# Performance work log

Measured on AMD Instinct MI355X. Metric: run time of the kernel, lower is better.

## Reference

```python
import jax, jax.numpy as jnp
import numpy as np

NX, NY = 384, 384
H = 1e-4
DT = 5e-9
NT = 192
STRIDE = 4
RHO = 1610.0
F0 = 2.0e6
T0 = 4e-7
AMP = 1e10
GAUSS_A = 5e6

C11_INIT, C22_INIT, C12_INIT = 1.3074e11, 1.15e10, 1.049e10
C16_INIT, C26_INIT, C66_INIT = 3.067e10, 3.75e9, 1.477e10
B11 = (5e10, 2.5e11); B22 = (5e9, 5e10); B12 = (5e9, 5e10)
B16 = (0.0, 6e10); B26 = (0.0, 2e10); B66 = (5e9, 3e10)


def setup_inputs() -> dict:
    # log-parameter fields, constant-initialized as in the module __init__
    full = lambda v: jnp.full((1, NX, NY), np.log(v), dtype=jnp.float32)
    log_C11 = full(C11_INIT)
    log_C22 = full(C22_INIT)
    log_C12 = full(C12_INIT)
    log_C16 = full(abs(C16_INIT) + 1e6)
    log_C26 = full(abs(C26_INIT) + 1e6)
    log_C66 = full(C66_INIT)
    # Gaussian point-load distribution centered at domain center
    Lx, Ly = H * (NX - 1), H * (NY - 1)
    x = np.linspace(-Lx / 2, Lx / 2, NX)
    y = np.linspace(-Ly / 2, Ly / 2, NY)
    X, Y = np.meshgrid(x, y, indexing='ij')
    gauss = (GAUSS_A / np.pi) * np.exp(-GAUSS_A * (X ** 2 + Y ** 2))
    # Ricker wavelet source signal over nt steps
    t = np.arange(NT) * DT
    tau = t - T0
    pft2 = (np.pi * F0 * tau) ** 2
    sig = AMP * (1.0 - 2.0 * pft2) * np.exp(-pft2)
    return {
        'log_C11': log_C11, 'log_C12': log_C12, 'log_C16': log_C16,
        'log_C22': log_C22, 'log_C26': log_C26, 'log_C66': log_C66,
        'gaussian_dist': jnp.asarray(gauss, dtype=jnp.float32),
        'source_signal': jnp.asarray(sig, dtype=jnp.float32),
    }


def _stencils(u, hinv2):
    # u: (B, nx, ny). Zero padding == fixed (u=0) boundary, matching conv2d_fixed.
    up = jnp.pad(u, ((0, 0), (1, 1), (1, 1)))
    d2x = (up[:, :-2, 1:-1] - 2.0 * u + up[:, 2:, 1:-1]) * hinv2
    d2y = (up[:, 1:-1, :-2] - 2.0 * u + up[:, 1:-1, 2:]) * hinv2
    dxy = 0.25 * (up[:, :-2, :-2] - up[:, :-2, 2:] - up[:, 2:, :-2] + up[:, 2:, 2:]) * hinv2
    return d2x, d2y, dxy


def _simulate(log_C11, log_C12, log_C16, log_C22, log_C26, log_C66,
              gaussian_dist, source_signal):
    clip = lambda lc, b: jnp.clip(jnp.exp(lc), b[0], b[1])
    C11 = clip(log_C11, B11); C22 = clip(log_C22, B22); C12 = clip(log_C12, B12)
    C16 = clip(log_C16, B16); C26 = clip(log_C26, B26); C66 = clip(log_C66, B66)
    hinv2 = jnp.float32(1.0 / (H * H))
    dt2 = jnp.float32(DT * DT)
    g = gaussian_dist[None]  # (1, nx, ny)
    C12p66 = C12 + C66

    def step(carry, sig_t):
        ux1, uy1, ux2, uy2 = carry
        dxx_x, dyy_x, dxy_x = _stencils(ux1, hinv2)
        dxx_y, dyy_y, dxy_y = _stencils(uy1, hinv2)
        Lux = (C11 * dxx_x + C66 * dyy_x + C12p66 * dxy_y
               + 2.0 * C16 * dxy_x + C16 * dxx_y + C26 * dyy_y)
        Luy = (C66 * dxx_y + C22 * dyy_y + C12p66 * dxy_x
               + C16 * dxx_x + C26 * dyy_x + 2.0 * C26 * dxy_y)
        # Ricker point source on the y-component (source_component='y')
        ax = Lux / RHO
        ay = (Luy + sig_t * g) / RHO
        ux_new = 2.0 * ux1 - ux2 + dt2 * ax
        uy_new = 2.0 * uy1 - uy2 + dt2 * ay
        return (ux_new, uy_new, ux1, uy1), (ux_new, uy_new)

    z = jnp.zeros((1, NX, NY), dtype=jnp.float32)
    _, (ux_all, uy_all) = jax.lax.scan(step, (z, z, z, z), source_signal)
    # subsample by primary_time_stride -> (1, nt//stride, nx, ny)
    ux_f = jnp.transpose(ux_all[STRIDE - 1::STRIDE], (1, 0, 2, 3))
    uy_f = jnp.transpose(uy_all[STRIDE - 1::STRIDE], (1, 0, 2, 3))
    return jnp.stack([ux_f, uy_f])  # (2, 1, nt_out, nx, ny)


def reference(log_C11, log_C12, log_C16, log_C22, log_C26, log_C66,
              gaussian_dist, source_signal):
    return _simulate(log_C11, log_C12, log_C16, log_C22, log_C26, log_C66,
                     gaussian_dist, source_signal)
```

## Files before the change

### kernel.cpp

```cpp
#include <hip/hip_runtime.h>


typedef float v2f __attribute__((ext_vector_type(2)));

#define NXg 384
#define NYg 384
#define NPT (NXg * NYg)
#define NFRAMES 48

#define OWN 24
#define HALO 12
#define TS 48
#define KSTEPS 12
#define NLAUNCH 16

#define H_   1e-4
#define DT_  5e-9
#define RHO_ 1610.0

#define B11_LO 5e10f
#define B11_HI 2.5e11f
#define B22_LO 5e9f
#define B22_HI 5e10f
#define B12_LO 5e9f
#define B12_HI 5e10f
#define B16_LO 0.0f
#define B16_HI 6e10f
#define B26_LO 0.0f
#define B26_HI 2e10f
#define B66_LO 5e9f
#define B66_HI 3e10f

static __device__ __constant__ float kScale  = (float)(DT_ * DT_ / (H_ * H_) / RHO_);
static __device__ __constant__ float kSrcScl = (float)(DT_ * DT_ / RHO_);

__device__ __forceinline__ float clipf(float v, float lo, float hi) {
    return fminf(fmaxf(v, lo), hi);
}
__device__ __forceinline__ v2f vfma(v2f a, v2f b, v2f c) {
    return __builtin_elementwise_fma(a, b, c);
}
__device__ __forceinline__ v2f vbc(float s) { v2f r; r[0] = s; r[1] = s; return r; }
__device__ __forceinline__ v2f vswap(v2f a) { return __builtin_shufflevector(a, a, 1, 0); }

#define LDS_BARRIER() asm volatile("s_waitcnt lgkmcnt(0)\n\ts_barrier" ::: "memory")


__global__ __launch_bounds__(256)
void setup_kernel(const float* __restrict__ lc11, const float* __restrict__ lc12,
                  const float* __restrict__ lc16, const float* __restrict__ lc22,
                  const float* __restrict__ lc26, const float* __restrict__ lc66,
                  const float* __restrict__ gauss, float* __restrict__ ws) {
    int i = blockIdx.x * blockDim.x + threadIdx.x;
    if (i >= NPT) return;
    float C11 = clipf(expf(lc11[i]), B11_LO, B11_HI);
    float C12 = clipf(expf(lc12[i]), B12_LO, B12_HI);
    float C16 = clipf(expf(lc16[i]), B16_LO, B16_HI);
    float C22 = clipf(expf(lc22[i]), B22_LO, B22_HI);
    float C26 = clipf(expf(lc26[i]), B26_LO, B26_HI);
    float C66 = clipf(expf(lc66[i]), B66_LO, B66_HI);
    float s = kScale;
    float4* C0 = (float4*)ws;
    float4* C1 = (float4*)(ws + 4 * (size_t)NPT);
    C0[i] = make_float4(C11 * s, C22 * s, (C12 + C66) * s, C16 * s);
    C1[i] = make_float4(C26 * s, C66 * s, gauss[i] * kSrcScl, 0.0f);
    float4* s0 = (float4*)(ws + 8 * (size_t)NPT);
    s0[i] = make_float4(0.0f, 0.0f, 0.0f, 0.0f);
}

__global__ __launch_bounds__(256, 1)
void fused_kernel(const float* __restrict__ ws, const float* __restrict__ sig,
                  const float4* __restrict__ inS, float4* __restrict__ outS,
                  float* __restrict__ out, int L) {
    __shared__ v2f sb[2][TS][TS + 1];

    const int tid = threadIdx.x;
    const int tx = tid >> 4;
    const int ty = tid & 15;
    const int r0 = 3 * tx;
    const int c0 = 3 * ty;
    const int gx0 = blockIdx.y * OWN - HALO;
    const int gy0 = blockIdx.x * OWN - HALO;

    const float4* __restrict__ C0 = (const float4*)ws;
    const float4* __restrict__ C1 = (const float4*)(ws + 4 * (size_t)NPT);

    v2f cur[9], old_[9];
    v2f ca[9], cb[9];
    float a12p66[9], a16[9], a26[9], gs[9];
    int gidx[9];

#pragma unroll
    for (int i = 0; i < 3; ++i) {
#pragma unroll
        for (int j = 0; j < 3; ++j) {
            int p = i * 3 + j;
            int gx = gx0 + r0 + i;
            int gy = gy0 + c0 + j;
            bool d = (unsigned)gx < (unsigned)NXg && (unsigned)gy < (unsigned)NYg;
            int g = d ? gx * NYg + gy : 0;
            gidx[p] = g;
            float4 st = d ? inS[g] : make_float4(0, 0, 0, 0);
            v2f c; c[0] = st.x; c[1] = st.y;
            v2f o; o[0] = st.z; o[1] = st.w;
            cur[p] = c; old_[p] = o;
            float4 k0 = d ? C0[g] : make_float4(0, 0, 0, 0);
            float4 k1 = d ? C1[g] : make_float4(0, 0, 0, 0);
            v2f t; t[0] = k0.x; t[1] = k1.y; ca[p] = t;
            v2f u; u[0] = k1.y; u[1] = k0.y; cb[p] = u;
            a12p66[p] = k0.z; a16[p] = k0.w; a26[p] = k1.x; gs[p] = k1.z;
        }
    }

    const int t0 = L * KSTEPS;
    float sigv[KSTEPS];
#pragma unroll
    for (int k = 0; k < KSTEPS; ++k) sigv[k] = sig[t0 + k];

    const int rm = (r0 > 0) ? r0 - 1 : 0;
    const int rp = (r0 + 3 < TS) ? r0 + 3 : TS - 1;
    const int cm = (c0 > 0) ? c0 - 1 : 0;
    const int cp = (c0 + 3 < TS) ? c0 + 3 : TS - 1;

    const bool owned = (tx >= 4) && (tx < 12) && (ty >= 4) && (ty < 12);

#pragma unroll
    for (int i = 0; i < 3; ++i)
#pragma unroll
        for (int j = 0; j < 3; ++j)
            sb[0][r0 + i][c0 + j] = cur[i * 3 + j];
    LDS_BARRIER();

    v2f c20; c20[0] = 2.0f; c20[1] = 0.0f;
    v2f c02; c02[0] = 0.0f; c02[1] = 2.0f;
    const v2f m2 = vbc(-2.0f);
    const v2f qt = vbc(0.25f);
    const v2f two = vbc(2.0f);

#pragma unroll 1
    for (int s = 1; s <= KSTEPS; ++s) {
        const v2f (*rb)[TS + 1] = sb[(s - 1) & 1];
        v2f (*wb)[TS + 1] = sb[s & 1];
        v2f vsig; vsig[0] = 0.0f; vsig[1] = sigv[s - 1];

        v2f v[5][5];
#pragma unroll
        for (int i = 0; i < 3; ++i)
#pragma unroll
            for (int j = 0; j < 3; ++j)
                v[i + 1][j + 1] = cur[i * 3 + j];
        v[0][0] = rb[rm][cm];  v[0][4] = rb[rm][cp];
        v[4][0] = rb[rp][cm];  v[4][4] = rb[rp][cp];
#pragma unroll
        for (int j = 0; j < 3; ++j) {
            v[0][j + 1] = rb[rm][c0 + j];
            v[4][j + 1] = rb[rp][c0 + j];
            v[j + 1][0] = rb[r0 + j][cm];
            v[j + 1][4] = rb[r0 + j][cp];
        }

        v2f dh[5][3];
#pragma unroll
        for (int i = 0; i < 5; ++i)
#pragma unroll
            for (int j = 0; j < 3; ++j)
                dh[i][j] = v[i][j + 2] - v[i][j];

#pragma unroll
        for (int i = 0; i < 3; ++i)
#pragma unroll
            for (int j = 0; j < 3; ++j) {
                int p = i * 3 + j;
                v2f c = v[i + 1][j + 1];
                v2f sxx = vfma(m2, c, v[i][j + 1] + v[i + 2][j + 1]);
                v2f syy = vfma(m2, c, v[i + 1][j] + v[i + 1][j + 2]);
                v2f sxy = qt * (dh[i + 2][j] - dh[i][j]);

                v2f t4 = vfma(c20, vbc(sxy[0]), vswap(sxx));
                v2f t5 = vfma(c02, vbc(sxy[1]), vswap(syy));
                v2f Lv = ca[p] * sxx;
                Lv = vfma(cb[p], syy, Lv);
                Lv = vfma(vbc(a12p66[p]), vswap(sxy), Lv);
                Lv = vfma(vbc(a16[p]), t4, Lv);
                Lv = vfma(vbc(a26[p]), t5, Lv);
                Lv = vfma(vsig, vbc(gs[p]), Lv);
                v2f n = vfma(two, c, Lv) - old_[p];
                old_[p] = c;
                cur[p] = n;
            }

        if ((s & 3) == 0 && owned) {
            int f = 3 * L + (s >> 2) - 1;
            float* oux = out + (size_t)f * NPT;
            float* ouy = out + (size_t)(NFRAMES + f) * NPT;
#pragma unroll
            for (int p = 0; p < 9; ++p) {
                oux[gidx[p]] = cur[p][0];
                ouy[gidx[p]] = cur[p][1];
            }
        }

#pragma unroll
        for (int i = 0; i < 3; ++i)
#pragma unroll
            for (int j = 0; j < 3; ++j)
                wb[r0 + i][c0 + j] = cur[i * 3 + j];
        LDS_BARRIER();
    }

    if (owned) {
#pragma unroll
        for (int p = 0; p < 9; ++p) {
            float4 st = make_float4(cur[p][0], cur[p][1], old_[p][0], old_[p][1]);
            outS[gidx[p]] = st;
        }
    }
}

extern "C" void kernel_launch(void* const* d_in, const int* in_sizes, int n_in,
                              void* d_out, int out_size, void* d_ws, size_t ws_size,
                              hipStream_t stream) {
    const float* lc11  = (const float*)d_in[0];
    const float* lc12  = (const float*)d_in[1];
    const float* lc16  = (const float*)d_in[2];
    const float* lc22  = (const float*)d_in[3];
    const float* lc26  = (const float*)d_in[4];
    const float* lc66  = (const float*)d_in[5];
    const float* gauss = (const float*)d_in[6];
    const float* sig   = (const float*)d_in[7];

    float* ws  = (float*)d_ws;
    float* out = (float*)d_out;

    setup_kernel<<<(NPT + 255) / 256, 256, 0, stream>>>(lc11, lc12, lc16, lc22,
                                                        lc26, lc66, gauss, ws);

    float4* set0 = (float4*)(ws + 8 * (size_t)NPT);
    float4* set1 = (float4*)(ws + 12 * (size_t)NPT);

    dim3 grid(NXg / OWN, NYg / OWN);
    for (int L = 0; L < NLAUNCH; ++L) {
        float4* iS = (L & 1) ? set1 : set0;
        float4* oS = (L & 1) ? set0 : set1;
        fused_kernel<<<grid, 256, 0, stream>>>(ws, sig, iS, oS, out, L);
    }
}
```

Before: 353.7 us.

## Replace per-epoch kernel launches with a persistent cooperative kernel using grid sync

The 16 separate launches of the temporally blocked stencil kernel become one cooperative persistent kernel that loops over epochs and uses grid.sync() between them. Owned cells keep their state in registers across epochs, and only halo cells reload from the global ping-pong state buffers. This targets launch overhead and the reload of coefficients and interior state on every launch. In exchange it depends on all 256 blocks being co-resident and adds grid-wide barrier latency.

After: 817.2 us. 131% more time.

```diff
diff --git a/kernel.cpp b/kernel.cpp
--- a/kernel.cpp
+++ b/kernel.cpp
@@ -1,4 +1,7 @@
 #include <hip/hip_runtime.h>
+#include <hip/hip_cooperative_groups.h>
+
+namespace cg = cooperative_groups;
 
 
 typedef float v2f __attribute__((ext_vector_type(2)));
@@ -12,7 +15,7 @@
 #define HALO 12
 #define TS 48
 #define KSTEPS 12
-#define NLAUNCH 16
+#define NEPOCH 16
 
 #define H_   1e-4
 #define DT_  5e-9
@@ -65,13 +68,16 @@
     C0[i] = make_float4(C11 * s, C22 * s, (C12 + C66) * s, C16 * s);
     C1[i] = make_float4(C26 * s, C66 * s, gauss[i] * kSrcScl, 0.0f);
     float4* s0 = (float4*)(ws + 8 * (size_t)NPT);
+    float4* s1 = (float4*)(ws + 12 * (size_t)NPT);
     s0[i] = make_float4(0.0f, 0.0f, 0.0f, 0.0f);
+    s1[i] = make_float4(0.0f, 0.0f, 0.0f, 0.0f);
 }
 
 __global__ __launch_bounds__(256, 1)
-void fused_kernel(const float* __restrict__ ws, const float* __restrict__ sig,
-                  const float4* __restrict__ inS, float4* __restrict__ outS,
-                  float* __restrict__ out, int L) {
+void persist_kernel(float* __restrict__ ws, const float* __restrict__ sig,
+                    float* __restrict__ out) {
+    cg::grid_group grid = cg::this_grid();
+
     __shared__ v2f sb[2][TS][TS + 1];
 
     const int tid = threadIdx.x;
@@ -84,11 +90,15 @@
 
     const float4* __restrict__ C0 = (const float4*)ws;
     const float4* __restrict__ C1 = (const float4*)(ws + 4 * (size_t)NPT);
+    float4* __restrict__ st[2];
+    st[0] = (float4*)(ws + 8 * (size_t)NPT);
+    st[1] = (float4*)(ws + 12 * (size_t)NPT);
 
     v2f cur[9], old_[9];
     v2f ca[9], cb[9];
     float a12p66[9], a16[9], a26[9], gs[9];
     int gidx[9];
+    bool dom[9];
 
 #pragma unroll
     for (int i = 0; i < 3; ++i) {
@@ -99,23 +109,16 @@
             int gy = gy0 + c0 + j;
             bool d = (unsigned)gx < (unsigned)NXg && (unsigned)gy < (unsigned)NYg;
             int g = d ? gx * NYg + gy : 0;
-            gidx[p] = g;
-            float4 st = d ? inS[g] : make_float4(0, 0, 0, 0);
-            v2f c; c[0] = st.x; c[1] = st.y;
-            v2f o; o[0] = st.z; o[1] = st.w;
-            cur[p] = c; old_[p] = o;
+            gidx[p] = g; dom[p] = d;
             float4 k0 = d ? C0[g] : make_float4(0, 0, 0, 0);
             float4 k1 = d ? C1[g] : make_float4(0, 0, 0, 0);
             v2f t; t[0] = k0.x; t[1] = k1.y; ca[p] = t;
             v2f u; u[0] = k1.y; u[1] = k0.y; cb[p] = u;
             a12p66[p] = k0.z; a16[p] = k0.w; a26[p] = k1.x; gs[p] = k1.z;
+            cur[p] = vbc(0.0f);
+            old_[p] = vbc(0.0f);
         }
     }
-
-    const int t0 = L * KSTEPS;
-    float sigv[KSTEPS];
-#pragma unroll
-    for (int k = 0; k < KSTEPS; ++k) sigv[k] = sig[t0 + k];
 
     const int rm = (r0 > 0) ? r0 - 1 : 0;
     const int rp = (r0 + 3 < TS) ? r0 + 3 : TS - 1;
@@ -123,13 +126,6 @@
     const int cp = (c0 + 3 < TS) ? c0 + 3 : TS - 1;
 
     const bool owned = (tx >= 4) && (tx < 12) && (ty >= 4) && (ty < 12);
-
-#pragma unroll
-    for (int i = 0; i < 3; ++i)
-#pragma unroll
-        for (int j = 0; j < 3; ++j)
-            sb[0][r0 + i][c0 + j] = cur[i * 3 + j];
-    LDS_BARRIER();
 
     v2f c20; c20[0] = 2.0f; c20[1] = 0.0f;
     v2f c02; c02[0] = 0.0f; c02[1] = 2.0f;
@@ -138,81 +134,111 @@
     const v2f two = vbc(2.0f);
 
 #pragma unroll 1
-    for (int s = 1; s <= KSTEPS; ++s) {
-        const v2f (*rb)[TS + 1] = sb[(s - 1) & 1];
-        v2f (*wb)[TS + 1] = sb[s & 1];
-        v2f vsig; vsig[0] = 0.0f; vsig[1] = sigv[s - 1];
-
-        v2f v[5][5];
+    for (int e = 0; e < NEPOCH; ++e) {
+        if (!owned) {
+            const float4* __restrict__ rs = st[(e + 1) & 1];
+#pragma unroll
+            for (int p = 0; p < 9; ++p) {
+                float4 s4 = dom[p] ? rs[gidx[p]] : make_float4(0, 0, 0, 0);
+                v2f c; c[0] = s4.x; c[1] = s4.y;
+                v2f o; o[0] = s4.z; o[1] = s4.w;
+                cur[p] = c; old_[p] = o;
+            }
+        }
+        const int t0 = e * KSTEPS;
+        float sigv[KSTEPS];
+#pragma unroll
+        for (int k = 0; k < KSTEPS; ++k) sigv[k] = sig[t0 + k];
+
 #pragma unroll
         for (int i = 0; i < 3; ++i)
 #pragma unroll
             for (int j = 0; j < 3; ++j)
-                v[i + 1][j + 1] = cur[i * 3 + j];
-        v[0][0] = rb[rm][cm];  v[0][4] = rb[rm][cp];
-        v[4][0] = rb[rp][cm];  v[4][4] = rb[rp][cp];
-#pragma unroll
-        for (int j = 0; j < 3; ++j) {
-            v[0][j + 1] = rb[rm][c0 + j];
-            v[4][j + 1] = rb[rp][c0 + j];
-            v[j + 1][0] = rb[r0 + j][cm];
-            v[j + 1][4] = rb[r0 + j][cp];
-        }
-
-        v2f dh[5][3];
-#pragma unroll
-        for (int i = 0; i < 5; ++i)
-#pragma unroll
-            for (int j = 0; j < 3; ++j)
-                dh[i][j] = v[i][j + 2] - v[i][j];
-
-#pragma unroll
-        for (int i = 0; i < 3; ++i)
+                sb[0][r0 + i][c0 + j] = cur[i * 3 + j];
+        LDS_BARRIER();
+
+#pragma unroll 1
+        for (int s = 1; s <= KSTEPS; ++s) {
+            const v2f (*rb)[TS + 1] = sb[(s - 1) & 1];
+            v2f (*wb)[TS + 1] = sb[s & 1];
+            v2f vsig; vsig[0] = 0.0f; vsig[1] = sigv[s - 1];
+
+            v2f v[5][5];
+#pragma unroll
+            for (int i = 0; i < 3; ++i)
+#pragma unroll
+                for (int j = 0; j < 3; ++j)
+                    v[i + 1][j + 1] = cur[i * 3 + j];
+            v[0][0] = rb[rm][cm];  v[0][4] = rb[rm][cp];
+            v[4][0] = rb[rp][cm];  v[4][4] = rb[rp][cp];
 #pragma unroll
             for (int j = 0; j < 3; ++j) {
-                int p = i * 3 + j;
-                v2f c = v[i + 1][j + 1];
-                v2f sxx = vfma(m2, c, v[i][j + 1] + v[i + 2][j + 1]);
-                v2f syy = vfma(m2, c, v[i + 1][j] + v[i + 1][j + 2]);
-                v2f sxy = qt * (dh[i + 2][j] - dh[i][j]);
-
-                v2f t4 = vfma(c20, vbc(sxy[0]), vswap(sxx));
-                v2f t5 = vfma(c02, vbc(sxy[1]), vswap(syy));
-                v2f Lv = ca[p] * sxx;
-                Lv = vfma(cb[p], syy, Lv);
-                Lv = vfma(vbc(a12p66[p]), vswap(sxy), Lv);
-                Lv = vfma(vbc(a16[p]), t4, Lv);
-                Lv = vfma(vbc(a26[p]), t5, Lv);
-                Lv = vfma(vsig, vbc(gs[p]), Lv);
-                v2f n = vfma(two, c, Lv) - old_[p];
-                old_[p] = c;
-                cur[p] = n;
-            }
-
-        if ((s & 3) == 0 && owned) {
-            int f = 3 * L + (s >> 2) - 1;
-            float* oux = out + (size_t)f * NPT;
-            float* ouy = out + (size_t)(NFRAMES + f) * NPT;
-#pragma unroll
-            for (int p = 0; p < 9; ++p) {
-                oux[gidx[p]] = cur[p][0];
-                ouy[gidx[p]] = cur[p][1];
-            }
-        }
-
-#pragma unroll
-        for (int i = 0; i < 3; ++i)
-#pragma unroll
-            for (int j = 0; j < 3; ++j)
-                wb[r0 + i][c0 + j] = cur[i * 3 + j];
-        LDS_BARRIER();
-    }
-
-    if (owned) {
-#pragma unroll
-        for (int p = 0; p < 9; ++p) {
-            float4 st = make_float4(cur[p][0], cur[p][1], old_[p][0], old_[p][1]);
-            outS[gidx[p]] = st;
+                v[0][j + 1] = rb[rm][c0 + j];
+                v[4][j + 1] = rb[rp][c0 + j];
+                v[j + 1][0] = rb[r0 + j][cm];
+                v[j + 1][4] = rb[r0 + j][cp];
+            }
+
+            v2f dh[5][3];
+#pragma unroll
+            for (int i = 0; i < 5; ++i)
+#pragma unroll
+                for (int j = 0; j < 3; ++j)
+                    dh[i][j] = v[i][j + 2] - v[i][j];
+
+#pragma unroll
+            for (int i = 0; i < 3; ++i)
+#pragma unroll
+                for (int j = 0; j < 3; ++j) {
+                    int p = i * 3 + j;
+                    v2f c = v[i + 1][j + 1];
+                    v2f sxx = vfma(m2, c, v[i][j + 1] + v[i + 2][j + 1]);
+                    v2f syy = vfma(m2, c, v[i + 1][j] + v[i + 1][j + 2]);
+                    v2f sxy = qt * (dh[i + 2][j] - dh[i][j]);
+
+                    v2f t4 = vfma(c20, vbc(sxy[0]), vswap(sxx));
+                    v2f t5 = vfma(c02, vbc(sxy[1]), vswap(syy));
+                    v2f Lv = ca[p] * sxx;
+                    Lv = vfma(cb[p], syy, Lv);
+                    Lv = vfma(vbc(a12p66[p]), vswap(sxy), Lv);
+                    Lv = vfma(vbc(a16[p]), t4, Lv);
+                    Lv = vfma(vbc(a26[p]), t5, Lv);
+                    Lv = vfma(vsig, vbc(gs[p]), Lv);
+                    v2f n = vfma(two, c, Lv) - old_[p];
+                    old_[p] = c;
+                    cur[p] = n;
+                }
+
+            if ((s & 3) == 0 && owned) {
+                int f = 3 * e + (s >> 2) - 1;
+                float* oux = out + (size_t)f * NPT;
+                float* ouy = out + (size_t)(NFRAMES + f) * NPT;
+#pragma unroll
+                for (int p = 0; p < 9; ++p) {
+                    oux[gidx[p]] = cur[p][0];
+                    ouy[gidx[p]] = cur[p][1];
+                }
+            }
+
+#pragma unroll
+            for (int i = 0; i < 3; ++i)
+#pragma unroll
+                for (int j = 0; j < 3; ++j)
+                    wb[r0 + i][c0 + j] = cur[i * 3 + j];
+            LDS_BARRIER();
+        }
+
+        if (e + 1 < NEPOCH) {
+            if (owned) {
+                float4* __restrict__ wsbuf = st[e & 1];
+#pragma unroll
+                for (int p = 0; p < 9; ++p) {
+                    float4 s4 = make_float4(cur[p][0], cur[p][1],
+                                            old_[p][0], old_[p][1]);
+                    wsbuf[gidx[p]] = s4;
+                }
+            }
+            grid.sync();
         }
     }
 }
@@ -235,13 +261,8 @@
     setup_kernel<<<(NPT + 255) / 256, 256, 0, stream>>>(lc11, lc12, lc16, lc22,
                                                         lc26, lc66, gauss, ws);
 
-    float4* set0 = (float4*)(ws + 8 * (size_t)NPT);
-    float4* set1 = (float4*)(ws + 12 * (size_t)NPT);
-
+    void* args[] = {(void*)&ws, (void*)&sig, (void*)&out};
     dim3 grid(NXg / OWN, NYg / OWN);
-    for (int L = 0; L < NLAUNCH; ++L) {
-        float4* iS = (L & 1) ? set1 : set0;
-        float4* oS = (L & 1) ? set0 : set1;
-        fused_kernel<<<grid, 256, 0, stream>>>(ws, sig, iS, oS, out, L);
-    }
-}
+    hipLaunchCooperativeKernel((void*)persist_kernel, grid, dim3(256), args, 0,
+                               stream);
+}
```

## Replace LDS tile exchange with per-wave row strips and DPP lane shifts

Applied to the files above, without the earlier changes.

The thread mapping changes from 3x3 point blocks to one column per lane, with each wavefront owning a 12-row strip. Neighbours along y now come from DPP lane shifts, and only the strip's boundary rows go through a small LDS buffer, with one barrier per step. This removes most LDS traffic and the scattered halo reads of the old shared tile. In exchange, 16 of every 64 lanes sit idle, and the code depends on DPP wave-shift support on the target hardware.

Result: slower. 391.4 us (+10.7%).

```diff
diff --git a/kernel.cpp b/kernel.cpp
--- a/kernel.cpp
+++ b/kernel.cpp
@@ -13,6 +13,7 @@
 #define TS 48
 #define KSTEPS 12
 #define NLAUNCH 16
+#define ROWS 12
 
 #define H_   1e-4
 #define DT_  5e-9
@@ -42,6 +43,23 @@
 }
 __device__ __forceinline__ v2f vbc(float s) { v2f r; r[0] = s; r[1] = s; return r; }
 __device__ __forceinline__ v2f vswap(v2f a) { return __builtin_shufflevector(a, a, 1, 0); }
+
+__device__ __forceinline__ float dpp_from_lo(float x) {
+    int v = __builtin_amdgcn_update_dpp(0, __builtin_bit_cast(int, x),
+                                        0x138, 0xf, 0xf, true);
+    return __builtin_bit_cast(float, v);
+}
+__device__ __forceinline__ float dpp_from_hi(float x) {
+    int v = __builtin_amdgcn_update_dpp(0, __builtin_bit_cast(int, x),
+                                        0x130, 0xf, 0xf, true);
+    return __builtin_bit_cast(float, v);
+}
+__device__ __forceinline__ v2f shiftL(v2f a) {
+    v2f r; r[0] = dpp_from_lo(a[0]); r[1] = dpp_from_lo(a[1]); return r;
+}
+__device__ __forceinline__ v2f shiftR(v2f a) {
+    v2f r; r[0] = dpp_from_hi(a[0]); r[1] = dpp_from_hi(a[1]); return r;
+}
 
 #define LDS_BARRIER() asm volatile("s_waitcnt lgkmcnt(0)\n\ts_barrier" ::: "memory")
 
@@ -72,44 +90,38 @@
 void fused_kernel(const float* __restrict__ ws, const float* __restrict__ sig,
                   const float4* __restrict__ inS, float4* __restrict__ outS,
                   float* __restrict__ out, int L) {
-    __shared__ v2f sb[2][TS][TS + 1];
+    __shared__ v2f xch[2][4][2][64];
 
     const int tid = threadIdx.x;
-    const int tx = tid >> 4;
-    const int ty = tid & 15;
-    const int r0 = 3 * tx;
-    const int c0 = 3 * ty;
-    const int gx0 = blockIdx.y * OWN - HALO;
-    const int gy0 = blockIdx.x * OWN - HALO;
+    const int w = tid >> 6;
+    const int c = tid & 63;
+    const int gx0 = (int)blockIdx.y * OWN - HALO;
+    const int gy = (int)blockIdx.x * OWN - HALO + c;
 
     const float4* __restrict__ C0 = (const float4*)ws;
     const float4* __restrict__ C1 = (const float4*)(ws + 4 * (size_t)NPT);
 
-    v2f cur[9], old_[9];
-    v2f ca[9], cb[9];
-    float a12p66[9], a16[9], a26[9], gs[9];
-    int gidx[9];
-
-#pragma unroll
-    for (int i = 0; i < 3; ++i) {
-#pragma unroll
-        for (int j = 0; j < 3; ++j) {
-            int p = i * 3 + j;
-            int gx = gx0 + r0 + i;
-            int gy = gy0 + c0 + j;
-            bool d = (unsigned)gx < (unsigned)NXg && (unsigned)gy < (unsigned)NYg;
-            int g = d ? gx * NYg + gy : 0;
-            gidx[p] = g;
-            float4 st = d ? inS[g] : make_float4(0, 0, 0, 0);
-            v2f c; c[0] = st.x; c[1] = st.y;
-            v2f o; o[0] = st.z; o[1] = st.w;
-            cur[p] = c; old_[p] = o;
-            float4 k0 = d ? C0[g] : make_float4(0, 0, 0, 0);
-            float4 k1 = d ? C1[g] : make_float4(0, 0, 0, 0);
-            v2f t; t[0] = k0.x; t[1] = k1.y; ca[p] = t;
-            v2f u; u[0] = k1.y; u[1] = k0.y; cb[p] = u;
-            a12p66[p] = k0.z; a16[p] = k0.w; a26[p] = k1.x; gs[p] = k1.z;
-        }
+    v2f cur[ROWS], old_[ROWS];
+    v2f ca[ROWS], cb[ROWS];
+    float a12p66[ROWS], a16[ROWS], a26[ROWS], gs[ROWS];
+    int g[ROWS];
+
+    const bool colOk = (c < TS) && ((unsigned)gy < (unsigned)NYg);
+#pragma unroll
+    for (int r = 0; r < ROWS; ++r) {
+        int gx = gx0 + ROWS * w + r;
+        bool d = colOk && ((unsigned)gx < (unsigned)NXg);
+        int gg = d ? gx * NYg + gy : 0;
+        g[r] = gg;
+        float4 st = d ? inS[gg] : make_float4(0, 0, 0, 0);
+        v2f cc; cc[0] = st.x; cc[1] = st.y;
+        v2f oo; oo[0] = st.z; oo[1] = st.w;
+        cur[r] = cc; old_[r] = oo;
+        float4 k0 = d ? C0[gg] : make_float4(0, 0, 0, 0);
+        float4 k1 = d ? C1[gg] : make_float4(0, 0, 0, 0);
+        v2f t; t[0] = k0.x; t[1] = k1.y; ca[r] = t;
+        v2f u; u[0] = k1.y; u[1] = k0.y; cb[r] = u;
+        a12p66[r] = k0.z; a16[r] = k0.w; a26[r] = k1.x; gs[r] = k1.z;
     }
 
     const int t0 = L * KSTEPS;
@@ -117,19 +129,10 @@
 #pragma unroll
     for (int k = 0; k < KSTEPS; ++k) sigv[k] = sig[t0 + k];
 
-    const int rm = (r0 > 0) ? r0 - 1 : 0;
-    const int rp = (r0 + 3 < TS) ? r0 + 3 : TS - 1;
-    const int cm = (c0 > 0) ? c0 - 1 : 0;
-    const int cp = (c0 + 3 < TS) ? c0 + 3 : TS - 1;
-
-    const bool owned = (tx >= 4) && (tx < 12) && (ty >= 4) && (ty < 12);
-
-#pragma unroll
-    for (int i = 0; i < 3; ++i)
-#pragma unroll
-        for (int j = 0; j < 3; ++j)
-            sb[0][r0 + i][c0 + j] = cur[i * 3 + j];
-    LDS_BARRIER();
+    const bool ownW = (w == 1) || (w == 2);
+    const bool ownC = (c >= HALO) && (c < HALO + OWN);
+    const int wa = (w > 0) ? w - 1 : w;
+    const int wb = (w < 3) ? w + 1 : w;
 
     v2f c20; c20[0] = 2.0f; c20[1] = 0.0f;
     v2f c02; c02[0] = 0.0f; c02[1] = 2.0f;
@@ -139,81 +142,69 @@
 
 #pragma unroll 1
     for (int s = 1; s <= KSTEPS; ++s) {
-        const v2f (*rb)[TS + 1] = sb[(s - 1) & 1];
-        v2f (*wb)[TS + 1] = sb[s & 1];
+        v2f (*xb)[2][64] = xch[s & 1];
+        xb[w][0][c] = cur[0];
+        xb[w][1][c] = cur[ROWS - 1];
+        LDS_BARRIER();
+        v2f Ba = xb[wa][1][c];
+        v2f Bb = xb[wb][0][c];
+        if (w == 0) Ba = vbc(0.0f);
+        if (w == 3) Bb = vbc(0.0f);
+
         v2f vsig; vsig[0] = 0.0f; vsig[1] = sigv[s - 1];
 
-        v2f v[5][5];
-#pragma unroll
-        for (int i = 0; i < 3; ++i)
-#pragma unroll
-            for (int j = 0; j < 3; ++j)
-                v[i + 1][j + 1] = cur[i * 3 + j];
-        v[0][0] = rb[rm][cm];  v[0][4] = rb[rm][cp];
-        v[4][0] = rb[rp][cm];  v[4][4] = rb[rp][cp];
-#pragma unroll
-        for (int j = 0; j < 3; ++j) {
-            v[0][j + 1] = rb[rm][c0 + j];
-            v[4][j + 1] = rb[rp][c0 + j];
-            v[j + 1][0] = rb[r0 + j][cm];
-            v[j + 1][4] = rb[r0 + j][cp];
+        v2f slA = shiftL(Ba), srA = shiftR(Ba);
+        v2f Dprev = slA - srA;
+        v2f below_prev = Ba;
+        v2f sl0 = shiftL(cur[0]), sr0 = shiftR(cur[0]);
+        v2f Dcur = sl0 - sr0;
+        v2f Scur = sl0 + sr0;
+
+#pragma unroll
+        for (int r = 0; r < ROWS; ++r) {
+            v2f nxt = (r < ROWS - 1) ? cur[r + 1] : Bb;
+            v2f sln = shiftL(nxt), srn = shiftR(nxt);
+            v2f Dnext = sln - srn;
+            v2f Snext = sln + srn;
+
+            v2f cc = cur[r];
+            v2f sxx = vfma(m2, cc, below_prev + nxt);
+            v2f syy = vfma(m2, cc, Scur);
+            v2f sxy = qt * (Dprev - Dnext);
+
+            v2f t4 = vfma(c20, vbc(sxy[0]), vswap(sxx));
+            v2f t5 = vfma(c02, vbc(sxy[1]), vswap(syy));
+            v2f Lv = ca[r] * sxx;
+            Lv = vfma(cb[r], syy, Lv);
+            Lv = vfma(vbc(a12p66[r]), vswap(sxy), Lv);
+            Lv = vfma(vbc(a16[r]), t4, Lv);
+            Lv = vfma(vbc(a26[r]), t5, Lv);
+            Lv = vfma(vsig, vbc(gs[r]), Lv);
+            v2f n = vfma(two, cc, Lv) - old_[r];
+
+            old_[r] = cc;
+            cur[r] = n;
+            below_prev = cc;
+            Dprev = Dcur; Dcur = Dnext; Scur = Snext;
         }
 
-        v2f dh[5][3];
-#pragma unroll
-        for (int i = 0; i < 5; ++i)
-#pragma unroll
-            for (int j = 0; j < 3; ++j)
-                dh[i][j] = v[i][j + 2] - v[i][j];
-
-#pragma unroll
-        for (int i = 0; i < 3; ++i)
-#pragma unroll
-            for (int j = 0; j < 3; ++j) {
-                int p = i * 3 + j;
-                v2f c = v[i + 1][j + 1];
-                v2f sxx = vfma(m2, c, v[i][j + 1] + v[i + 2][j + 1]);
-                v2f syy = vfma(m2, c, v[i + 1][j] + v[i + 1][j + 2]);
-                v2f sxy = qt * (dh[i + 2][j] - dh[i][j]);
-
-                v2f t4 = vfma(c20, vbc(sxy[0]), vswap(sxx));
-                v2f t5 = vfma(c02, vbc(sxy[1]), vswap(syy));
-                v2f Lv = ca[p] * sxx;
-                Lv = vfma(cb[p], syy, Lv);
-                Lv = vfma(vbc(a12p66[p]), vswap(sxy), Lv);
-                Lv = vfma(vbc(a16[p]), t4, Lv);
-                Lv = vfma(vbc(a26[p]), t5, Lv);
-                Lv = vfma(vsig, vbc(gs[p]), Lv);
-                v2f n = vfma(two, c, Lv) - old_[p];
-                old_[p] = c;
-                cur[p] = n;
-            }
-
-        if ((s & 3) == 0 && owned) {
+        if ((s & 3) == 0 && ownW && ownC) {
             int f = 3 * L + (s >> 2) - 1;
             float* oux = out + (size_t)f * NPT;
             float* ouy = out + (size_t)(NFRAMES + f) * NPT;
 #pragma unroll
-            for (int p = 0; p < 9; ++p) {
-                oux[gidx[p]] = cur[p][0];
-                ouy[gidx[p]] = cur[p][1];
+            for (int r = 0; r < ROWS; ++r) {
+                oux[g[r]] = cur[r][0];
+                ouy[g[r]] = cur[r][1];
             }
         }
-
-#pragma unroll
-        for (int i = 0; i < 3; ++i)
-#pragma unroll
-            for (int j = 0; j < 3; ++j)
-                wb[r0 + i][c0 + j] = cur[i * 3 + j];
-        LDS_BARRIER();
-    }
-
-    if (owned) {
-#pragma unroll
-        for (int p = 0; p < 9; ++p) {
-            float4 st = make_float4(cur[p][0], cur[p][1], old_[p][0], old_[p][1]);
-            outS[gidx[p]] = st;
-        }
+    }
+
+    if (ownW && ownC) {
+#pragma unroll
+        for (int r = 0; r < ROWS; ++r)
+            outS[g[r]] = make_float4(cur[r][0], cur[r][1],
+                                     old_[r][0], old_[r][1]);
     }
 }
 
```

## Use 512-thread blocks with 2x3 points per thread and a taller halo tile

Applied to the files above, without the earlier changes.

Each block now runs 512 threads over a 64x48 LDS tile. Each thread owns 2x3 points instead of 3x3, and the row halo grows from 12 to 20 so the thread grid divides the tile evenly. The goal is twice the waves per CU and fewer registers per thread, to hide LDS and ALU latency in the time-stepping loop. The cost is about a third more redundant halo computation per block. The final step's LDS write and barrier are also skipped, since nothing reads them.

After: 373.2 us. 1.05x slower.

```diff
diff --git a/kernel.cpp b/kernel.cpp
--- a/kernel.cpp
+++ b/kernel.cpp
@@ -9,10 +9,13 @@
 #define NFRAMES 48
 
 #define OWN 24
-#define HALO 12
-#define TS 48
+#define HALOR 20
+#define HALOC 12
+#define TSR 64
+#define TSC 48
 #define KSTEPS 12
 #define NLAUNCH 16
+#define SCOL 49
 
 #define H_   1e-4
 #define DT_  5e-9
@@ -68,30 +71,30 @@
     s0[i] = make_float4(0.0f, 0.0f, 0.0f, 0.0f);
 }
 
-__global__ __launch_bounds__(256, 1)
+__global__ __launch_bounds__(512)
 void fused_kernel(const float* __restrict__ ws, const float* __restrict__ sig,
                   const float4* __restrict__ inS, float4* __restrict__ outS,
                   float* __restrict__ out, int L) {
-    __shared__ v2f sb[2][TS][TS + 1];
+    __shared__ v2f sb[2][TSR][SCOL];
 
     const int tid = threadIdx.x;
-    const int tx = tid >> 4;
-    const int ty = tid & 15;
-    const int r0 = 3 * tx;
-    const int c0 = 3 * ty;
-    const int gx0 = blockIdx.y * OWN - HALO;
-    const int gy0 = blockIdx.x * OWN - HALO;
+    const int rg = tid >> 4;
+    const int cg = tid & 15;
+    const int r0 = 2 * rg;
+    const int c0 = 3 * cg;
+    const int gx0 = (int)blockIdx.y * OWN - HALOR;
+    const int gy0 = (int)blockIdx.x * OWN - HALOC;
 
     const float4* __restrict__ C0 = (const float4*)ws;
     const float4* __restrict__ C1 = (const float4*)(ws + 4 * (size_t)NPT);
 
-    v2f cur[9], old_[9];
-    v2f ca[9], cb[9];
-    float a12p66[9], a16[9], a26[9], gs[9];
-    int gidx[9];
-
-#pragma unroll
-    for (int i = 0; i < 3; ++i) {
+    v2f cur[6], old_[6];
+    v2f ca[6], cb[6];
+    float a12p66[6], a16[6], a26[6], gs[6];
+    int gidx[6];
+
+#pragma unroll
+    for (int i = 0; i < 2; ++i) {
 #pragma unroll
         for (int j = 0; j < 3; ++j) {
             int p = i * 3 + j;
@@ -118,14 +121,14 @@
     for (int k = 0; k < KSTEPS; ++k) sigv[k] = sig[t0 + k];
 
     const int rm = (r0 > 0) ? r0 - 1 : 0;
-    const int rp = (r0 + 3 < TS) ? r0 + 3 : TS - 1;
+    const int rp = (r0 + 2 < TSR) ? r0 + 2 : TSR - 1;
     const int cm = (c0 > 0) ? c0 - 1 : 0;
-    const int cp = (c0 + 3 < TS) ? c0 + 3 : TS - 1;
-
-    const bool owned = (tx >= 4) && (tx < 12) && (ty >= 4) && (ty < 12);
-
-#pragma unroll
-    for (int i = 0; i < 3; ++i)
+    const int cp = (c0 + 3 < TSC) ? c0 + 3 : TSC - 1;
+
+    const bool owned = (rg >= 10) && (rg < 22) && (cg >= 4) && (cg < 12);
+
+#pragma unroll
+    for (int i = 0; i < 2; ++i)
 #pragma unroll
         for (int j = 0; j < 3; ++j)
             sb[0][r0 + i][c0 + j] = cur[i * 3 + j];
@@ -139,42 +142,43 @@
 
 #pragma unroll 1
     for (int s = 1; s <= KSTEPS; ++s) {
-        const v2f (*rb)[TS + 1] = sb[(s - 1) & 1];
-        v2f (*wb)[TS + 1] = sb[s & 1];
+        const v2f (*rb)[SCOL] = sb[(s - 1) & 1];
+        v2f (*wb)[SCOL] = sb[s & 1];
         v2f vsig; vsig[0] = 0.0f; vsig[1] = sigv[s - 1];
 
-        v2f v[5][5];
-#pragma unroll
-        for (int i = 0; i < 3; ++i)
+        v2f v[4][5];
+#pragma unroll
+        for (int i = 0; i < 2; ++i)
 #pragma unroll
             for (int j = 0; j < 3; ++j)
                 v[i + 1][j + 1] = cur[i * 3 + j];
         v[0][0] = rb[rm][cm];  v[0][4] = rb[rm][cp];
-        v[4][0] = rb[rp][cm];  v[4][4] = rb[rp][cp];
+        v[3][0] = rb[rp][cm];  v[3][4] = rb[rp][cp];
 #pragma unroll
         for (int j = 0; j < 3; ++j) {
             v[0][j + 1] = rb[rm][c0 + j];
-            v[4][j + 1] = rb[rp][c0 + j];
-            v[j + 1][0] = rb[r0 + j][cm];
-            v[j + 1][4] = rb[r0 + j][cp];
-        }
-
-        v2f dh[5][3];
-#pragma unroll
-        for (int i = 0; i < 5; ++i)
+            v[3][j + 1] = rb[rp][c0 + j];
+        }
+        v[1][0] = rb[r0][cm];      v[1][4] = rb[r0][cp];
+        v[2][0] = rb[r0 + 1][cm];  v[2][4] = rb[r0 + 1][cp];
+
+        v2f dh[4][3];
+#pragma unroll
+        for (int i = 0; i < 4; ++i)
 #pragma unroll
             for (int j = 0; j < 3; ++j)
                 dh[i][j] = v[i][j + 2] - v[i][j];
 
 #pragma unroll
-        for (int i = 0; i < 3; ++i)
+        for (int i = 0; i < 2; ++i)
 #pragma unroll
             for (int j = 0; j < 3; ++j) {
                 int p = i * 3 + j;
-                v2f c = v[i + 1][j + 1];
-                v2f sxx = vfma(m2, c, v[i][j + 1] + v[i + 2][j + 1]);
-                v2f syy = vfma(m2, c, v[i + 1][j] + v[i + 1][j + 2]);
-                v2f sxy = qt * (dh[i + 2][j] - dh[i][j]);
+                int pi = i + 1, pj = j + 1;
+                v2f c = v[pi][pj];
+                v2f sxx = vfma(m2, c, v[pi - 1][pj] + v[pi + 1][pj]);
+                v2f syy = vfma(m2, c, v[pi][pj - 1] + v[pi][pj + 1]);
+                v2f sxy = qt * (dh[pi + 1][j] - dh[pi - 1][j]);
 
                 v2f t4 = vfma(c20, vbc(sxy[0]), vswap(sxx));
                 v2f t5 = vfma(c02, vbc(sxy[1]), vswap(syy));
@@ -194,23 +198,25 @@
             float* oux = out + (size_t)f * NPT;
             float* ouy = out + (size_t)(NFRAMES + f) * NPT;
 #pragma unroll
-            for (int p = 0; p < 9; ++p) {
+            for (int p = 0; p < 6; ++p) {
                 oux[gidx[p]] = cur[p][0];
                 ouy[gidx[p]] = cur[p][1];
             }
         }
 
-#pragma unroll
-        for (int i = 0; i < 3; ++i)
-#pragma unroll
-            for (int j = 0; j < 3; ++j)
-                wb[r0 + i][c0 + j] = cur[i * 3 + j];
-        LDS_BARRIER();
+        if (s < KSTEPS) {
+#pragma unroll
+            for (int i = 0; i < 2; ++i)
+#pragma unroll
+                for (int j = 0; j < 3; ++j)
+                    wb[r0 + i][c0 + j] = cur[i * 3 + j];
+            LDS_BARRIER();
+        }
     }
 
     if (owned) {
 #pragma unroll
-        for (int p = 0; p < 9; ++p) {
+        for (int p = 0; p < 6; ++p) {
             float4 st = make_float4(cur[p][0], cur[p][1], old_[p][0], old_[p][1]);
             outS[gidx[p]] = st;
         }
@@ -238,10 +244,10 @@
     float4* set0 = (float4*)(ws + 8 * (size_t)NPT);
     float4* set1 = (float4*)(ws + 12 * (size_t)NPT);
 
-    dim3 grid(NXg / OWN, NYg / OWN);
+    dim3 grid(NYg / OWN, NXg / OWN);
     for (int L = 0; L < NLAUNCH; ++L) {
         float4* iS = (L & 1) ? set1 : set0;
         float4* oS = (L & 1) ? set0 : set1;
-        fused_kernel<<<grid, 256, 0, stream>>>(ws, sig, iS, oS, out, L);
-    }
-}
+        fused_kernel<<<grid, 512, 0, stream>>>(ws, sig, iS, oS, out, L);
+    }
+}
```
